# Kernel tuning notes

Hardware: AMD Instinct MI355X
Metric: run time of the kernel (lower is better)

The kernel has to match this reference:

```python
import jax, jax.numpy as jnp
import numpy as np

D_MODEL = 256   # per-head dim in this module
N_HEAD = 8
B, S = 4, 2048
NEG_INF = -1e9  # large negative in place of -inf for numerical safety


def setup_inputs() -> dict:
    key = jax.random.key(0)
    ks = jax.random.split(key, 8)
    d, h = D_MODEL, N_HEAD
    sc = 1.0 / np.sqrt(d)
    return {
        "Q": jax.random.normal(ks[0], (B, S, d), jnp.float32),
        "mask": jax.random.randint(ks[1], (B, S), 0, 2, jnp.int32),
        "WQ_w": jax.random.normal(ks[2], (h * d, d), jnp.float32) * sc,
        "WQ_b": jnp.zeros((h * d,), jnp.float32),
        "WK_w": jax.random.normal(ks[3], (h * d, d), jnp.float32) * sc,
        "WK_b": jnp.zeros((h * d,), jnp.float32),
        "WV_w": jax.random.normal(ks[4], (h * d, d), jnp.float32) * sc,
        "WV_b": jnp.zeros((h * d,), jnp.float32),
        "WO_w": jax.random.normal(ks[5], (d, h * d), jnp.float32) * sc,
        "WO_b": jnp.zeros((d,), jnp.float32),
        "ln_g": jnp.ones((d,), jnp.float32),
        "ln_b": jnp.zeros((d,), jnp.float32),
    }


def reference(Q, mask, WQ_w, WQ_b, WK_w, WK_b, WV_w, WV_b, WO_w, WO_b, ln_g, ln_b):
    b, s, d = Q.shape
    h = N_HEAD
    # projections (torch Linear: x @ W.T + b), split into heads: [b, h, s, d]
    q = (Q @ WQ_w.T + WQ_b).reshape(b, s, h, d).transpose(0, 2, 1, 3)
    k = (Q @ WK_w.T + WK_b).reshape(b, s, h, d).transpose(0, 2, 1, 3)
    v = (Q @ WV_w.T + WV_b).reshape(b, s, h, d).transpose(0, 2, 1, 3)
    # scaled dot-product scores [b, h, q, k]
    scores = jnp.einsum('bhqd,bhkd->bhqk', q, k) / jnp.sqrt(jnp.asarray(d, Q.dtype))
    key_mask = (mask != 0)[:, None, None, :]  # [b,1,1,k]
    scores = jnp.where(key_mask, scores, NEG_INF)
    alpha = jax.nn.softmax(scores, axis=-1)
    out = jnp.einsum('bhqk,bhkd->bhqd', alpha, v)
    out = out.transpose(0, 2, 1, 3).reshape(b, s, h * d)
    out = out @ WO_w.T + WO_b + Q  # dropout is identity in eval
    # LayerNorm over last dim
    mu = out.mean(-1, keepdims=True)
    var = out.var(-1, keepdims=True)
    return (out - mu) / jnp.sqrt(var + 1e-5) * ln_g + ln_b
```

## Files before the change

### kernel.cpp

```cpp
#include <hip/hip_runtime.h>
#include <cstddef>
#include <cstdint>

#define SQ 2048
#define DH 256
#define NH 8
#define BATCH 4
#define MROWS (BATCH*SQ)
#define HID (NH*DH)

typedef __attribute__((ext_vector_type(8)))  short bf16x8;
typedef __attribute__((ext_vector_type(16))) float f32x16;

typedef __attribute__((address_space(1))) const unsigned char gbuf_t;
typedef __attribute__((address_space(3))) unsigned char lbuf_t;

__device__ __forceinline__ void gl_lds16(const void* g, void* l) {
  __builtin_amdgcn_global_load_lds((gbuf_t*)g, (lbuf_t*)l, 16, 0, 0);
}

__device__ __forceinline__ unsigned short f2bf(float f) {
  unsigned u = __float_as_uint(f);
  unsigned r = (u + 0x7FFFu + ((u >> 16) & 1u)) >> 16;
  return (unsigned short)r;
}
__device__ __forceinline__ unsigned pk2(float a, float b) {
  return (unsigned)f2bf(a) | ((unsigned)f2bf(b) << 16);
}
__device__ __forceinline__ float fexp2(float x) {
  float r;
  asm("v_exp_f32 %0, %1" : "=v"(r) : "v"(x));
  return r;
}
__device__ __forceinline__ f32x16 zero16() {
  f32x16 v;
#pragma unroll
  for (int i = 0; i < 16; ++i) v[i] = 0.0f;
  return v;
}

__global__ void __launch_bounds__(256) cvt_kernel(
    const float* __restrict__ X,  const float* __restrict__ Wq,
    const float* __restrict__ Wk, const float* __restrict__ Wv,
    const float* __restrict__ Wo,
    unsigned short* __restrict__ Xb,  unsigned short* __restrict__ Wqb,
    unsigned short* __restrict__ Wkb, unsigned short* __restrict__ Wvb,
    unsigned short* __restrict__ Wob)
{
  int bid = blockIdx.x;
  const float* src; unsigned short* dst; size_t off;
  if      (bid < 512) { src = X;  dst = Xb;  off = (size_t)bid * 4096; }
  else if (bid < 640) { src = Wq; dst = Wqb; off = (size_t)(bid - 512) * 4096; }
  else if (bid < 768) { src = Wk; dst = Wkb; off = (size_t)(bid - 640) * 4096; }
  else if (bid < 896) { src = Wv; dst = Wvb; off = (size_t)(bid - 768) * 4096; }
  else                { src = Wo; dst = Wob; off = (size_t)(bid - 896) * 4096; }
  int tid = threadIdx.x;
#pragma unroll
  for (int k = 0; k < 4; ++k) {
    size_t idx = off + ((size_t)k * 256 + tid) * 4;
    float4 v = *(const float4*)(src + idx);
    uint2 o; o.x = pk2(v.x, v.y); o.y = pk2(v.z, v.w);
    *(uint2*)(dst + idx) = o;
  }
}

__global__ void __launch_bounds__(256) qkv_kernel(
    const unsigned short* __restrict__ Xbf,
    const unsigned short* __restrict__ Wqb,
    const unsigned short* __restrict__ Wkb,
    const unsigned short* __restrict__ Wvb,
    const float* __restrict__ bq, const float* __restrict__ bk, const float* __restrict__ bv,
    unsigned short* __restrict__ q_ws, unsigned short* __restrict__ k_ws,
    unsigned short* __restrict__ vt_ws)
{
  __shared__ unsigned char TA[65536];
  __shared__ unsigned char TB[65536];
  const int tid = threadIdx.x, w = tid >> 6, l = tid & 63;
  const int h = l >> 5, t = l & 31;
  const int wm = w >> 1, wn = w & 1;
  const int z = blockIdx.z;
  const int m0 = (z == 2) ? blockIdx.y * 128 : blockIdx.x * 128;
  const int n0 = (z == 2) ? blockIdx.x * 128 : blockIdx.y * 128;
  const unsigned short* Asrc = (z == 2) ? Wvb : Xbf;
  const unsigned short* Bsrc = (z == 0) ? Wqb : (z == 1) ? Wkb : Xbf;

  const int rowo = l >> 5;
  const int bin  = (l & 31) * 16;
#pragma unroll
  for (int i2 = 0; i2 < 16; ++i2) {
    int i = 16 * w + i2;
    int row = 2 * i + rowo;
    gl_lds16((const unsigned char*)(Asrc + (size_t)(m0 + row) * 256) + (bin ^ ((row & 15) << 4)),
             &TA[i * 1024]);
  }
#pragma unroll
  for (int i2 = 0; i2 < 16; ++i2) {
    int i = 16 * w + i2;
    int row = 2 * i + rowo;
    gl_lds16((const unsigned char*)(Bsrc + (size_t)(n0 + row) * 256) + (bin ^ ((row & 15) << 4)),
             &TB[i * 1024]);
  }
  __syncthreads();

  f32x16 acc00 = zero16(), acc01 = zero16(), acc10 = zero16(), acc11 = zero16();
  const int swz = (t & 15) << 4;
#pragma unroll
  for (int kc = 0; kc < 16; ++kc) {
    int kb = (32 * kc + 16 * h) ^ swz;
    bf16x8 a0 = *(const bf16x8*)&TA[(size_t)(64 * wm + t) * 512 + kb];
    bf16x8 a1 = *(const bf16x8*)&TA[(size_t)(64 * wm + 32 + t) * 512 + kb];
    bf16x8 b0 = *(const bf16x8*)&TB[(size_t)(64 * wn + t) * 512 + kb];
    bf16x8 b1 = *(const bf16x8*)&TB[(size_t)(64 * wn + 32 + t) * 512 + kb];
    acc00 = __builtin_amdgcn_mfma_f32_32x32x16_bf16(a0, b0, acc00, 0, 0, 0);
    acc01 = __builtin_amdgcn_mfma_f32_32x32x16_bf16(a0, b1, acc01, 0, 0, 0);
    acc10 = __builtin_amdgcn_mfma_f32_32x32x16_bf16(a1, b0, acc10, 0, 0, 0);
    acc11 = __builtin_amdgcn_mfma_f32_32x32x16_bf16(a1, b1, acc11, 0, 0, 0);
  }

  if (z < 2) {
    unsigned short* outp = z ? k_ws : q_ws;
    const float* bias = z ? bk : bq;
    float bn0 = bias[n0 + 64 * wn + t];
    float bn1 = bias[n0 + 64 * wn + 32 + t];
#pragma unroll
    for (int mt = 0; mt < 2; ++mt) {
#pragma unroll
      for (int nt = 0; nt < 2; ++nt) {
        int n = n0 + 64 * wn + 32 * nt + t;
        int headn = n >> 8, d = n & 255;
        float bb = nt ? bn1 : bn0;
        const f32x16& A = (mt == 0) ? (nt == 0 ? acc00 : acc01) : (nt == 0 ? acc10 : acc11);
#pragma unroll
        for (int r = 0; r < 16; ++r) {
          int m = m0 + 64 * wm + 32 * mt + (r & 3) + 8 * (r >> 2) + 4 * h;
          int batch = m >> 11, s = m & 2047;
          outp[(((size_t)batch * NH + headn) * SQ + s) * DH + d] = f2bf(A[r] + bb);
        }
      }
    }
  } else {
#pragma unroll
    for (int mt = 0; mt < 2; ++mt) {
#pragma unroll
      for (int r = 0; r < 16; ++r) {
        int j = m0 + 64 * wm + 32 * mt + (r & 3) + 8 * (r >> 2) + 4 * h;
        float bj = bv[j];
        int headj = j >> 8, jl = j & 255;
#pragma unroll
        for (int nt = 0; nt < 2; ++nt) {
          int sall = n0 + 64 * wn + 32 * nt + t;
          int batch = sall >> 11, ss = sall & 2047;
          const f32x16& A = (mt == 0) ? (nt == 0 ? acc00 : acc01) : (nt == 0 ? acc10 : acc11);
          vt_ws[((size_t)batch * NH + headj) * DH * SQ + (size_t)jl * SQ + ss] = f2bf(A[r] + bj);
        }
      }
    }
  }
}

__global__ void __launch_bounds__(512, 2) attn_kernel(
    const unsigned short* __restrict__ q_ws,
    const unsigned short* __restrict__ k_ws,
    const unsigned short* __restrict__ vt_ws,
    const int* __restrict__ mask,
    unsigned short* __restrict__ o_ws)
{
  __shared__ unsigned char KT[2][32768];
  __shared__ unsigned char VT[2][32768];
  __shared__ float MB[2048];

  const int tid = threadIdx.x, w = tid >> 6, l = tid & 63;
  const int h = l >> 5, t = l & 31;
  const int bid = blockIdx.x;
  const int xcd = bid & 7, slot = bid >> 3;
  const int bh = xcd * 4 + (slot >> 3);
  const int qt = slot & 7;
  const int b = bh >> 3, head = bh & 7;
  const int q0 = qt * 256;

  const float SC2 = 0.0625f * 1.44269504f;
  const float THR = 11.54f;

  {
    const int* mrow = mask + b * SQ;
    for (int i = tid; i < SQ; i += 512) MB[i] = mrow[i] ? 0.0f : -1.0e9f;
  }

  const unsigned short* kplane = k_ws + (size_t)bh * SQ * DH;
  const unsigned short* vplane = vt_ws + (size_t)bh * DH * SQ;

  bf16x8 qf[16];
  {
    const unsigned short* qb = q_ws + ((size_t)bh * SQ + (q0 + 32 * w + t)) * DH + 8 * h;
#pragma unroll
    for (int kc = 0; kc < 16; ++kc) qf[kc] = *(const bf16x8*)(qb + 16 * kc);
  }

  const int krow_o = l >> 5, kcol = (l & 31) * 16;
  const int vrow_o = l >> 3, vcol = (l & 7) * 16;

  {
#pragma unroll
    for (int i = 0; i < 4; ++i) {
      int j = 4 * w + i;
      int row = 2 * j + krow_o;
      gl_lds16((const unsigned char*)(kplane + (size_t)row * DH) + (kcol ^ ((row & 15) << 4)),
               &KT[0][j * 1024]);
    }
#pragma unroll
    for (int i = 0; i < 4; ++i) {
      int j = 4 * w + i;
      int row = 8 * j + vrow_o;
      gl_lds16((const unsigned char*)(vplane + (size_t)row * SQ) + (vcol ^ ((row & 7) << 4)),
               &VT[0][j * 1024]);
    }
  }
  __syncthreads();

  f32x16 o[8];
#pragma unroll
  for (int i = 0; i < 8; ++i) o[i] = zero16();
  float m_run = -3.0e38f, l_run = 0.0f;

  const int swzK = (t & 15) << 4;
  const int swzV = (t & 7) << 4;

  int cur = 0;
  for (int kb = 0; kb < SQ; kb += 64) {
    const int nxt = cur ^ 1;
    if (kb + 64 < SQ) {
#pragma unroll
      for (int i = 0; i < 4; ++i) {
        int j = 4 * w + i;
        int row = 2 * j + krow_o;
        gl_lds16((const unsigned char*)(kplane + (size_t)(kb + 64 + row) * DH) + (kcol ^ ((row & 15) << 4)),
                 &KT[nxt][j * 1024]);
      }
#pragma unroll
      for (int i = 0; i < 4; ++i) {
        int j = 4 * w + i;
        int row = 8 * j + vrow_o;
        gl_lds16((const unsigned char*)(vplane + (size_t)row * SQ + kb + 64) + (vcol ^ ((row & 7) << 4)),
                 &VT[nxt][j * 1024]);
      }
    }

    f32x16 sa0 = zero16(), sa1 = zero16();
    __builtin_amdgcn_s_setprio(1);
#pragma unroll
    for (int kc = 0; kc < 16; ++kc) {
      int kbb = (32 * kc + 16 * h) ^ swzK;
      bf16x8 a0 = *(const bf16x8*)&KT[cur][(size_t)t * 512 + kbb];
      bf16x8 a1 = *(const bf16x8*)&KT[cur][(size_t)(32 + t) * 512 + kbb];
      sa0 = __builtin_amdgcn_mfma_f32_32x32x16_bf16(a0, qf[kc], sa0, 0, 0, 0);
      sa1 = __builtin_amdgcn_mfma_f32_32x32x16_bf16(a1, qf[kc], sa1, 0, 0, 0);
    }
    __builtin_amdgcn_s_setprio(0);

#pragma unroll
    for (int g = 0; g < 4; ++g) {
      float4 m0v = *(const float4*)&MB[kb + 4 * h + 8 * g];
      float4 m1v = *(const float4*)&MB[kb + 32 + 4 * h + 8 * g];
      sa0[4*g+0] = sa0[4*g+0] * SC2 + m0v.x;
      sa0[4*g+1] = sa0[4*g+1] * SC2 + m0v.y;
      sa0[4*g+2] = sa0[4*g+2] * SC2 + m0v.z;
      sa0[4*g+3] = sa0[4*g+3] * SC2 + m0v.w;
      sa1[4*g+0] = sa1[4*g+0] * SC2 + m1v.x;
      sa1[4*g+1] = sa1[4*g+1] * SC2 + m1v.y;
      sa1[4*g+2] = sa1[4*g+2] * SC2 + m1v.z;
      sa1[4*g+3] = sa1[4*g+3] * SC2 + m1v.w;
    }
    f32x16 mm;
#pragma unroll
    for (int r = 0; r < 16; ++r) mm[r] = fmaxf(sa0[r], sa1[r]);
#pragma unroll
    for (int s = 8; s >= 1; s >>= 1) {
#pragma unroll
      for (int r = 0; r < 8; ++r) {
        if (r < s) mm[r] = fmaxf(mm[r], mm[r + s]);
      }
    }
    float tm = fmaxf(mm[0], __shfl_xor(mm[0], 32, 64));

    if (__builtin_expect(!__all(tm <= m_run + THR), 0)) {
      float m_new = fmaxf(m_run, tm);
      float rf = fexp2(m_run - m_new);
      m_run = m_new;
      l_run *= rf;
#pragma unroll
      for (int r = 0; r < 16; ++r) {
        float rr = __shfl(rf, (r & 3) + 8 * (r >> 2) + 4 * h, 64);
#pragma unroll
        for (int db = 0; db < 8; ++db) o[db][r] *= rr;
      }
    }

    float ssum = 0.0f;
#pragma unroll
    for (int ks = 0; ks < 4; ++ks) {
      const f32x16& P = (ks < 2) ? sa0 : sa1;
      const int base = 8 * (ks & 1);
      float e0 = fexp2(P[base + 0] - m_run);
      float e1 = fexp2(P[base + 1] - m_run);
      float e2 = fexp2(P[base + 2] - m_run);
      float e3 = fexp2(P[base + 3] - m_run);
      float e4 = fexp2(P[base + 4] - m_run);
      float e5 = fexp2(P[base + 5] - m_run);
      float e6 = fexp2(P[base + 6] - m_run);
      float e7 = fexp2(P[base + 7] - m_run);
      unsigned lo0, lo1, hi0, hi1;
      asm("v_cvt_pk_bf16_f32 %0, %1, %2" : "=v"(lo0) : "v"(e0), "v"(e1));
      asm("v_cvt_pk_bf16_f32 %0, %1, %2" : "=v"(lo1) : "v"(e2), "v"(e3));
      asm("v_cvt_pk_bf16_f32 %0, %1, %2" : "=v"(hi0) : "v"(e4), "v"(e5));
      asm("v_cvt_pk_bf16_f32 %0, %1, %2" : "=v"(hi1) : "v"(e6), "v"(e7));
      unsigned s0 = h ? lo0 : hi0;
      unsigned s1 = h ? lo1 : hi1;
      unsigned x0 = (unsigned)__shfl_xor((int)s0, 32, 64);
      unsigned x1 = (unsigned)__shfl_xor((int)s1, 32, 64);
      union { unsigned u[4]; bf16x8 v; } pu;
      pu.u[0] = h ? x0 : lo0;
      pu.u[1] = h ? x1 : lo1;
      pu.u[2] = h ? hi0 : x0;
      pu.u[3] = h ? hi1 : x1;
      bf16x8 pav = pu.v;
      ssum += ((e0 + e1) + (e2 + e3)) + ((e4 + e5) + (e6 + e7));
      __builtin_amdgcn_s_setprio(1);
#pragma unroll
      for (int db = 0; db < 8; ++db) {
        bf16x8 bv = *(const bf16x8*)&VT[cur][(size_t)(32 * db + t) * 128 + ((32 * ks + 16 * h) ^ swzV)];
        o[db] = __builtin_amdgcn_mfma_f32_32x32x16_bf16(pav, bv, o[db], 0, 0, 0);
      }
      __builtin_amdgcn_s_setprio(0);
    }
    float ls = ssum + __shfl_xor(ssum, 32, 64);
    l_run += ls;

    __syncthreads();
    cur = nxt;
  }

  float linv = 1.0f / l_run;
  unsigned short* ob = o_ws + (size_t)b * SQ * HID + (size_t)head * DH;
#pragma unroll
  for (int r = 0; r < 16; ++r) {
    int rowr = (r & 3) + 8 * (r >> 2) + 4 * h;
    float li = __shfl(linv, rowr, 64);
    int s = q0 + 32 * w + rowr;
    unsigned short* orow = ob + (size_t)s * HID;
#pragma unroll
    for (int db = 0; db < 8; ++db)
      orow[32 * db + t] = f2bf(o[db][r] * li);
  }
}

__global__ void __launch_bounds__(256) oproj_kernel(
    const unsigned short* __restrict__ Abf,
    const unsigned short* __restrict__ Wob,
    float* __restrict__ tmp)
{
  __shared__ unsigned char TA[8192];
  __shared__ unsigned char TB[16384];
  const int tid = threadIdx.x, w = tid >> 6, l = tid & 63;
  const int h = l >> 5, t = l & 31;
  const int wm = w >> 1, wn = w & 1;
  const int m0 = blockIdx.x * 64, n0 = blockIdx.y * 128;
  const int arow_o = l >> 3, ab_in = (l & 7) * 16;
  const int swz = (t & 7) << 4;

  f32x16 acc0 = zero16(), acc1 = zero16();
  for (int chunk = 0; chunk < 32; ++chunk) {
    __syncthreads();
#pragma unroll
    for (int i2 = 0; i2 < 2; ++i2) {
      int i = 2 * w + i2;
      int row = 8 * i + arow_o;
      gl_lds16((const unsigned char*)(Abf + (size_t)(m0 + row) * HID + chunk * 64) + (ab_in ^ ((row & 7) << 4)),
               &TA[i * 1024]);
    }
#pragma unroll
    for (int i2 = 0; i2 < 4; ++i2) {
      int i = 4 * w + i2;
      int row = 8 * i + arow_o;
      gl_lds16((const unsigned char*)(Wob + (size_t)(n0 + row) * HID + chunk * 64) + (ab_in ^ ((row & 7) << 4)),
               &TB[i * 1024]);
    }
    __syncthreads();
#pragma unroll
    for (int kc = 0; kc < 4; ++kc) {
      int kbb = (32 * kc + 16 * h) ^ swz;
      bf16x8 a  = *(const bf16x8*)&TA[(size_t)(32 * wm + t) * 128 + kbb];
      bf16x8 b0 = *(const bf16x8*)&TB[(size_t)(64 * wn + t) * 128 + kbb];
      bf16x8 b1 = *(const bf16x8*)&TB[(size_t)(64 * wn + 32 + t) * 128 + kbb];
      acc0 = __builtin_amdgcn_mfma_f32_32x32x16_bf16(a, b0, acc0, 0, 0, 0);
      acc1 = __builtin_amdgcn_mfma_f32_32x32x16_bf16(a, b1, acc1, 0, 0, 0);
    }
  }
#pragma unroll
  for (int nt = 0; nt < 2; ++nt) {
    const f32x16& A = nt ? acc1 : acc0;
    int n = n0 + 64 * wn + 32 * nt + t;
#pragma unroll
    for (int r = 0; r < 16; ++r) {
      int m = m0 + 32 * wm + (r & 3) + 8 * (r >> 2) + 4 * h;
      tmp[(size_t)m * DH + n] = A[r];
    }
  }
}

__global__ void __launch_bounds__(256) ln_kernel(
    const float* __restrict__ tmp, const float* __restrict__ bo,
    const float* __restrict__ Xin, const float* __restrict__ g,
    const float* __restrict__ be, float* __restrict__ out)
{
  const int tid = threadIdx.x, w = tid >> 6, lane = tid & 63;
  const int row = blockIdx.x * 4 + w;
  float4 v  = ((const float4*)(tmp + (size_t)row * DH))[lane];
  float4 qv = ((const float4*)(Xin + (size_t)row * DH))[lane];
  float4 bb = ((const float4*)bo)[lane];
  v.x += qv.x + bb.x; v.y += qv.y + bb.y; v.z += qv.z + bb.z; v.w += qv.w + bb.w;
  float s1 = v.x + v.y + v.z + v.w;
  float s2 = v.x * v.x + v.y * v.y + v.z * v.z + v.w * v.w;
#pragma unroll
  for (int off = 1; off < 64; off <<= 1) {
    s1 += __shfl_xor(s1, off, 64);
    s2 += __shfl_xor(s2, off, 64);
  }
  float mean = s1 * (1.0f / 256.0f);
  float var = s2 * (1.0f / 256.0f) - mean * mean;
  float rstd = rsqrtf(var + 1e-5f);
  float4 gg = ((const float4*)g)[lane];
  float4 b2 = ((const float4*)be)[lane];
  float4 o;
  o.x = (v.x - mean) * rstd * gg.x + b2.x;
  o.y = (v.y - mean) * rstd * gg.y + b2.y;
  o.z = (v.z - mean) * rstd * gg.z + b2.z;
  o.w = (v.w - mean) * rstd * gg.w + b2.w;
  ((float4*)(out + (size_t)row * DH))[lane] = o;
}

extern "C" void kernel_launch(void* const* d_in, const int* in_sizes, int n_in,
                              void* d_out, int out_size, void* d_ws, size_t ws_size,
                              hipStream_t stream) {
  const float* Q    = (const float*)d_in[0];
  const int*   mask = (const int*)  d_in[1];
  const float* WQ_w = (const float*)d_in[2];
  const float* WQ_b = (const float*)d_in[3];
  const float* WK_w = (const float*)d_in[4];
  const float* WK_b = (const float*)d_in[5];
  const float* WV_w = (const float*)d_in[6];
  const float* WV_b = (const float*)d_in[7];
  const float* WO_w = (const float*)d_in[8];
  const float* WO_b = (const float*)d_in[9];
  const float* ln_g = (const float*)d_in[10];
  const float* ln_b = (const float*)d_in[11];
  float* out = (float*)d_out;

  uint8_t* ws = (uint8_t*)d_ws;
  const size_t MB1 = 1048576;
  unsigned short* Xb   = (unsigned short*)(ws + 0 * MB1);
  unsigned short* Wqb  = (unsigned short*)(ws + 4 * MB1);
  unsigned short* Wkb  = (unsigned short*)(ws + 5 * MB1);
  unsigned short* Wvb  = (unsigned short*)(ws + 6 * MB1);
  unsigned short* Wob  = (unsigned short*)(ws + 7 * MB1);
  unsigned short* q_ws = (unsigned short*)(ws + 8 * MB1);
  unsigned short* k_ws = (unsigned short*)(ws + 40 * MB1);
  unsigned short* vtws = (unsigned short*)(ws + 72 * MB1);
  unsigned short* o_ws = (unsigned short*)(ws + 104 * MB1);
  float*          tmpf = (float*)         (ws + 136 * MB1);

  cvt_kernel<<<1024, 256, 0, stream>>>(Q, WQ_w, WK_w, WV_w, WO_w, Xb, Wqb, Wkb, Wvb, Wob);
  qkv_kernel<<<dim3(64, 16, 3), 256, 0, stream>>>(Xb, Wqb, Wkb, Wvb, WQ_b, WK_b, WV_b,
                                                  q_ws, k_ws, vtws);
  attn_kernel<<<dim3(256), 512, 0, stream>>>(q_ws, k_ws, vtws, mask, o_ws);
  oproj_kernel<<<dim3(128, 2), 256, 0, stream>>>(o_ws, Wob, tmpf);
  ln_kernel<<<2048, 256, 0, stream>>>(tmpf, WO_b, Q, ln_g, ln_b, out);
}
```

Baseline: 295.1 us.

## Fuse output projection with residual add and LayerNorm into one kernel

Merges the O-projection GEMM and the LayerNorm kernel. Each block now covers 32 full rows across all 256 output columns, so row statistics can be reduced in registers and shared memory without writing an fp32 intermediate to global memory. This removes one kernel launch and the round trip of the temporary buffer. In exchange, each block reloads the whole Wo tile per chunk into a larger LDS buffer, and the grid of 256 blocks has fewer MFMA tiles per wave.

New measurement: 297.2 us. About the same (+0.7%).

```diff
diff --git a/kernel.cpp b/kernel.cpp
--- a/kernel.cpp
+++ b/kernel.cpp
@@ -353,89 +353,88 @@
   }
 }
 
-__global__ void __launch_bounds__(256) oproj_kernel(
+__global__ void __launch_bounds__(256) oproj_ln_kernel(
     const unsigned short* __restrict__ Abf,
     const unsigned short* __restrict__ Wob,
-    float* __restrict__ tmp)
+    const float* __restrict__ bo, const float* __restrict__ Xin,
+    const float* __restrict__ g, const float* __restrict__ be,
+    float* __restrict__ out)
 {
-  __shared__ unsigned char TA[8192];
-  __shared__ unsigned char TB[16384];
+  __shared__ unsigned char TA[4096];
+  __shared__ unsigned char TB[32768];
+  __shared__ float RS1[4][32], RS2[4][32];
   const int tid = threadIdx.x, w = tid >> 6, l = tid & 63;
   const int h = l >> 5, t = l & 31;
-  const int wm = w >> 1, wn = w & 1;
-  const int m0 = blockIdx.x * 64, n0 = blockIdx.y * 128;
+  const int m0 = blockIdx.x * 32;
   const int arow_o = l >> 3, ab_in = (l & 7) * 16;
   const int swz = (t & 7) << 4;
 
   f32x16 acc0 = zero16(), acc1 = zero16();
   for (int chunk = 0; chunk < 32; ++chunk) {
     __syncthreads();
-#pragma unroll
-    for (int i2 = 0; i2 < 2; ++i2) {
-      int i = 2 * w + i2;
-      int row = 8 * i + arow_o;
+    {
+      int row = 8 * w + arow_o;
       gl_lds16((const unsigned char*)(Abf + (size_t)(m0 + row) * HID + chunk * 64) + (ab_in ^ ((row & 7) << 4)),
-               &TA[i * 1024]);
-    }
-#pragma unroll
-    for (int i2 = 0; i2 < 4; ++i2) {
-      int i = 4 * w + i2;
-      int row = 8 * i + arow_o;
-      gl_lds16((const unsigned char*)(Wob + (size_t)(n0 + row) * HID + chunk * 64) + (ab_in ^ ((row & 7) << 4)),
-               &TB[i * 1024]);
+               &TA[w * 1024]);
+    }
+#pragma unroll
+    for (int i2 = 0; i2 < 8; ++i2) {
+      int j = 8 * w + i2;
+      int row = 8 * j + arow_o;
+      gl_lds16((const unsigned char*)(Wob + (size_t)row * HID + chunk * 64) + (ab_in ^ ((row & 7) << 4)),
+               &TB[j * 1024]);
     }
     __syncthreads();
 #pragma unroll
     for (int kc = 0; kc < 4; ++kc) {
       int kbb = (32 * kc + 16 * h) ^ swz;
-      bf16x8 a  = *(const bf16x8*)&TA[(size_t)(32 * wm + t) * 128 + kbb];
-      bf16x8 b0 = *(const bf16x8*)&TB[(size_t)(64 * wn + t) * 128 + kbb];
-      bf16x8 b1 = *(const bf16x8*)&TB[(size_t)(64 * wn + 32 + t) * 128 + kbb];
+      bf16x8 a  = *(const bf16x8*)&TA[(size_t)t * 128 + kbb];
+      bf16x8 b0 = *(const bf16x8*)&TB[(size_t)(64 * w + t) * 128 + kbb];
+      bf16x8 b1 = *(const bf16x8*)&TB[(size_t)(64 * w + 32 + t) * 128 + kbb];
       acc0 = __builtin_amdgcn_mfma_f32_32x32x16_bf16(a, b0, acc0, 0, 0, 0);
       acc1 = __builtin_amdgcn_mfma_f32_32x32x16_bf16(a, b1, acc1, 0, 0, 0);
     }
   }
-#pragma unroll
-  for (int nt = 0; nt < 2; ++nt) {
-    const f32x16& A = nt ? acc1 : acc0;
-    int n = n0 + 64 * wn + 32 * nt + t;
-#pragma unroll
-    for (int r = 0; r < 16; ++r) {
-      int m = m0 + 32 * wm + (r & 3) + 8 * (r >> 2) + 4 * h;
-      tmp[(size_t)m * DH + n] = A[r];
-    }
-  }
-}
-
-__global__ void __launch_bounds__(256) ln_kernel(
-    const float* __restrict__ tmp, const float* __restrict__ bo,
-    const float* __restrict__ Xin, const float* __restrict__ g,
-    const float* __restrict__ be, float* __restrict__ out)
-{
-  const int tid = threadIdx.x, w = tid >> 6, lane = tid & 63;
-  const int row = blockIdx.x * 4 + w;
-  float4 v  = ((const float4*)(tmp + (size_t)row * DH))[lane];
-  float4 qv = ((const float4*)(Xin + (size_t)row * DH))[lane];
-  float4 bb = ((const float4*)bo)[lane];
-  v.x += qv.x + bb.x; v.y += qv.y + bb.y; v.z += qv.z + bb.z; v.w += qv.w + bb.w;
-  float s1 = v.x + v.y + v.z + v.w;
-  float s2 = v.x * v.x + v.y * v.y + v.z * v.z + v.w * v.w;
-#pragma unroll
-  for (int off = 1; off < 64; off <<= 1) {
-    s1 += __shfl_xor(s1, off, 64);
-    s2 += __shfl_xor(s2, off, 64);
-  }
-  float mean = s1 * (1.0f / 256.0f);
-  float var = s2 * (1.0f / 256.0f) - mean * mean;
-  float rstd = rsqrtf(var + 1e-5f);
-  float4 gg = ((const float4*)g)[lane];
-  float4 b2 = ((const float4*)be)[lane];
-  float4 o;
-  o.x = (v.x - mean) * rstd * gg.x + b2.x;
-  o.y = (v.y - mean) * rstd * gg.y + b2.y;
-  o.z = (v.z - mean) * rstd * gg.z + b2.z;
-  o.w = (v.w - mean) * rstd * gg.w + b2.w;
-  ((float4*)(out + (size_t)row * DH))[lane] = o;
+
+  const int c0 = 64 * w + t, c1 = 64 * w + 32 + t;
+  float bb0 = bo[c0], bb1 = bo[c1];
+  float gc0 = g[c0],  gc1 = g[c1];
+  float bc0 = be[c0], bc1 = be[c1];
+#pragma unroll
+  for (int r = 0; r < 16; ++r) {
+    int row = m0 + (r & 3) + 8 * (r >> 2) + 4 * h;
+    acc0[r] += bb0 + Xin[(size_t)row * DH + c0];
+    acc1[r] += bb1 + Xin[(size_t)row * DH + c1];
+  }
+
+#pragma unroll
+  for (int r = 0; r < 16; ++r) {
+    float p1 = acc0[r] + acc1[r];
+    float p2 = acc0[r] * acc0[r] + acc1[r] * acc1[r];
+#pragma unroll
+    for (int off = 1; off < 32; off <<= 1) {
+      p1 += __shfl_xor(p1, off, 64);
+      p2 += __shfl_xor(p2, off, 64);
+    }
+    if (t == 0) {
+      int rl = (r & 3) + 8 * (r >> 2) + 4 * h;
+      RS1[w][rl] = p1; RS2[w][rl] = p2;
+    }
+  }
+  __syncthreads();
+
+#pragma unroll
+  for (int r = 0; r < 16; ++r) {
+    int rl = (r & 3) + 8 * (r >> 2) + 4 * h;
+    float s1 = (RS1[0][rl] + RS1[1][rl]) + (RS1[2][rl] + RS1[3][rl]);
+    float s2 = (RS2[0][rl] + RS2[1][rl]) + (RS2[2][rl] + RS2[3][rl]);
+    float mean = s1 * (1.0f / 256.0f);
+    float var  = s2 * (1.0f / 256.0f) - mean * mean;
+    float rstd = rsqrtf(var + 1e-5f);
+    size_t rowo = (size_t)(m0 + rl) * DH;
+    out[rowo + c0] = (acc0[r] - mean) * rstd * gc0 + bc0;
+    out[rowo + c1] = (acc1[r] - mean) * rstd * gc1 + bc1;
+  }
 }
 
 extern "C" void kernel_launch(void* const* d_in, const int* in_sizes, int n_in,
@@ -466,12 +465,10 @@
   unsigned short* k_ws = (unsigned short*)(ws + 40 * MB1);
   unsigned short* vtws = (unsigned short*)(ws + 72 * MB1);
   unsigned short* o_ws = (unsigned short*)(ws + 104 * MB1);
-  float*          tmpf = (float*)         (ws + 136 * MB1);
 
   cvt_kernel<<<1024, 256, 0, stream>>>(Q, WQ_w, WK_w, WV_w, WO_w, Xb, Wqb, Wkb, Wvb, Wob);
   qkv_kernel<<<dim3(64, 16, 3), 256, 0, stream>>>(Xb, Wqb, Wkb, Wvb, WQ_b, WK_b, WV_b,
                                                   q_ws, k_ws, vtws);
   attn_kernel<<<dim3(256), 512, 0, stream>>>(q_ws, k_ws, vtws, mask, o_ws);
-  oproj_kernel<<<dim3(128, 2), 256, 0, stream>>>(o_ws, Wob, tmpf);
-  ln_kernel<<<2048, 256, 0, stream>>>(tmpf, WO_b, Q, ln_g, ln_b, out);
-}
+  oproj_ln_kernel<<<dim3(256), 256, 0, stream>>>(o_ws, Wob, WO_b, Q, ln_g, ln_b, out);
+}
```
